# Performance work log

Hardware: AMD Instinct MI355X
Metric: run time of the kernel (lower is better)

The kernel has to match this reference:

```python
import jax, jax.numpy as jnp
import numpy as np

B, C, N = 16, 128, 2048  # batch, channels (SA_Layer(128)), num points


def setup_inputs() -> dict:
    key = jax.random.key(0)
    ks = jax.random.split(key, 6)
    x = jax.random.normal(ks[0], (B, C, N), jnp.float32)
    wq = jax.random.normal(ks[1], (C // 4, C), jnp.float32) * 0.05  # shared q/k 1x1 conv, no bias
    wv = jax.random.normal(ks[2], (C, C), jnp.float32) * 0.05
    bv = jax.random.normal(ks[3], (C,), jnp.float32) * 0.05
    wt = jax.random.normal(ks[4], (C, C), jnp.float32) * 0.05
    bt = jax.random.normal(ks[5], (C,), jnp.float32) * 0.05
    gamma = jnp.ones((C,), jnp.float32)   # BatchNorm1d weight
    beta = jnp.zeros((C,), jnp.float32)   # BatchNorm1d bias
    bn_mean = jnp.zeros((C,), jnp.float32)  # running mean (eval mode)
    bn_var = jnp.ones((C,), jnp.float32)    # running var (eval mode)
    return dict(x=x, wq=wq, wv=wv, bv=bv, wt=wt, bt=bt,
                gamma=gamma, beta=beta, bn_mean=bn_mean, bn_var=bn_var)


def reference(x, wq, wv, bv, wt, bt, gamma, beta, bn_mean, bn_var):
    EPS = 1e-9
    BN_EPS = 1e-5
    # q_conv and k_conv share weights (tied in __init__)
    x_q = jnp.einsum('dc,bcn->bnd', wq, x)               # [B, N, C/4]
    x_k = jnp.einsum('dc,bcn->bdn', wq, x)               # [B, C/4, N]
    energy = jnp.einsum('bnd,bdm->bnm', x_q, x_k)        # [B, N, N]
    attn = jax.nn.softmax(energy, axis=-1)
    # offset-attention renormalization: divide by column sum
    attn = attn / (EPS + attn.sum(axis=1, keepdims=True))
    x_v = jnp.einsum('dc,bcn->bdn', wv, x) + bv[None, :, None]   # [B, C, N]
    x_r = jnp.einsum('bdn,bnm->bdm', x_v, attn)                  # [B, C, N]
    t = jnp.einsum('dc,bcn->bdn', wt, x - x_r) + bt[None, :, None]
    # BatchNorm1d (eval mode) + ReLU
    t = (t - bn_mean[None, :, None]) * jax.lax.rsqrt(bn_var + BN_EPS)[None, :, None]
    t = t * gamma[None, :, None] + beta[None, :, None]
    return x + jax.nn.relu(t)
```

## Files before the change

### kernel.cpp

```cpp
#include <hip/hip_runtime.h>
#include <hip/hip_bf16.h>
#include <math.h>

#define BB 16
#define CC 128
#define NN 2048
#define CQ 32

typedef __attribute__((ext_vector_type(8))) short bf16x8;
typedef __attribute__((ext_vector_type(4))) float f32x4;
typedef __attribute__((ext_vector_type(16))) float f32x16;
typedef unsigned char uchar;

__device__ __forceinline__ ushort f2b(float f) {
    __hip_bfloat16 h = __float2bfloat16(f);
    return *reinterpret_cast<ushort*>(&h);
}
__device__ __forceinline__ float b2f(ushort u) {
    union { unsigned u; float f; } v; v.u = ((unsigned)u) << 16;
    return v.f;
}
__device__ __forceinline__ uint f2q4(float a, float b, float c, float d) {
    int r = __builtin_amdgcn_cvt_pk_fp8_f32(a, b, 0, false);
    r = __builtin_amdgcn_cvt_pk_fp8_f32(c, d, r, true);
    return (uint)r;
}
__device__ __forceinline__ bf16x8 as_b8(uint4 u) {
    union { uint4 u; bf16x8 b; } v; v.u = u; return v.b;
}
__device__ __forceinline__ bf16x8 as_b8_2(uint2 a, uint2 b) {
    return as_b8(make_uint4(a.x, a.y, b.x, b.y));
}
__device__ __forceinline__ float fexp2(float x) {
    return __builtin_amdgcn_exp2f(x);
}
union U2L { uint2 u; long l; };

#define OFF_VB  524288
#define OFF_RSI 4718592

#define QSCALE 1.2011224087864498f

__global__ __launch_bounds__(256) void k_proj(const float* __restrict__ x,
        const float* __restrict__ wq, const float* __restrict__ wv,
        const float* __restrict__ bv, ushort* __restrict__ Qt, uchar* __restrict__ Vb) {
    __shared__ ushort Wl[160][136];
    __shared__ ushort Xs[64][136];
    int bid = (blockIdx.x & 7) * 64 + (blockIdx.x >> 3);
    int b  = bid >> 5;
    int n0 = (bid & 31) << 6;
    int tid = threadIdx.x;
    #pragma unroll
    for (int k = 0; k < 20; ++k) {
        int idx = k * 256 + tid;
        int r = idx >> 5, c4 = (idx & 31) << 2;
        const float* srcw = (r < 32) ? (wq + r * 128 + c4) : (wv + (r - 32) * 128 + c4);
        float4 w4 = *(const float4*)srcw;
        float s = (r < 32) ? QSCALE : 1.0f;
        *(ushort4*)&Wl[r][c4] = make_ushort4(f2b(w4.x * s), f2b(w4.y * s),
                                             f2b(w4.z * s), f2b(w4.w * s));
    }
    const float* xb = x + (size_t)b * CC * NN;
    for (int idx = tid; idx < 2048; idx += 256) {
        int c = idx >> 4, n4 = (idx & 15) << 2;
        float4 xv = *(const float4*)&xb[c * NN + n0 + n4];
        Xs[n4][c]     = f2b(xv.x);
        Xs[n4 + 1][c] = f2b(xv.y);
        Xs[n4 + 2][c] = f2b(xv.z);
        Xs[n4 + 3][c] = f2b(xv.w);
    }
    __syncthreads();
    int w = tid >> 6, l = tid & 63, lr = l & 15, lg = l >> 4;
    f32x4 zero = {0.f, 0.f, 0.f, 0.f};
    int nn = n0 + w * 16 + lr;
    for (int dt = 0; dt < 10; ++dt) {
        f32x4 acc = zero;
        #pragma unroll
        for (int k = 0; k < 4; ++k) {
            bf16x8 a  = *(const bf16x8*)&Wl[dt * 16 + lr][k * 32 + lg * 8];
            bf16x8 bx = *(const bf16x8*)&Xs[w * 16 + lr][k * 32 + lg * 8];
            acc = __builtin_amdgcn_mfma_f32_16x16x32_bf16(a, bx, acc, 0, 0, 0);
        }
        if (dt < 2) {
            ushort4 p = make_ushort4(f2b(acc[0]), f2b(acc[1]), f2b(acc[2]), f2b(acc[3]));
            *(ushort4*)&Qt[(size_t)(b * NN + nn) * CQ + dt * 16 + lg * 4] = p;
        } else {
            union { uint u; uchar c[4]; } q;
            int vd = (dt - 2) * 16 + lg * 4;
            q.u = f2q4(acc[0] + bv[vd], acc[1] + bv[vd + 1],
                       acc[2] + bv[vd + 2], acc[3] + bv[vd + 3]);
            #pragma unroll
            for (int i = 0; i < 4; ++i)
                Vb[(size_t)(b * CC + vd + i) * NN + nn] = q.c[i];
        }
    }
}

__global__ __launch_bounds__(512) void k_rowstats(const ushort* __restrict__ Qt,
        float* __restrict__ RSI) {
    __shared__ ushort Qm[128][36];
    __shared__ float Sred[2][64];
    int bid = (blockIdx.x & 7) * 64 + (blockIdx.x >> 3);
    int b  = bid >> 5;
    int n0 = (bid & 31) << 6;
    int tid = threadIdx.x;
    int w = tid >> 6, l = tid & 63, lr = l & 15, lg = l >> 4;
    int wn = w & 3, wm = w >> 2;
    const ushort* Qtb = Qt + (size_t)b * NN * CQ;
    bf16x8 aq = *(const bf16x8*)&Qtb[(size_t)(n0 + wn * 16 + lr) * CQ + lg * 8];
    int sr = tid >> 2, sc = (tid & 3) * 8;
    uint4 q0 = *(const uint4*)&Qtb[(size_t)sr * CQ + sc];
    float S[4] = {0.f, 0.f, 0.f, 0.f};
    f32x4 zero = {0.f, 0.f, 0.f, 0.f};
    for (int t = 0; t < 16; ++t) {
        __syncthreads();
        *(uint4*)&Qm[sr][sc] = q0;
        __syncthreads();
        if (t < 15)
            q0 = *(const uint4*)&Qtb[(size_t)((t + 1) * 128 + sr) * CQ + sc];
        #pragma unroll
        for (int mi = 0; mi < 4; ++mi) {
            bf16x8 bq = *(const bf16x8*)&Qm[(wm * 4 + mi) * 16 + lr][lg * 8];
            f32x4 e = __builtin_amdgcn_mfma_f32_16x16x32_bf16(aq, bq, zero, 0, 0, 0);
            S[0] += fexp2(e[0]); S[1] += fexp2(e[1]);
            S[2] += fexp2(e[2]); S[3] += fexp2(e[3]);
        }
    }
    #pragma unroll
    for (int d = 1; d < 16; d <<= 1) {
        #pragma unroll
        for (int i = 0; i < 4; ++i) S[i] += __shfl_xor(S[i], d);
    }
    if (lr == 0) {
        #pragma unroll
        for (int i = 0; i < 4; ++i) Sred[wm][wn * 16 + lg * 4 + i] = S[i];
    }
    __syncthreads();
    if (tid < 64)
        RSI[b * NN + n0 + tid] = 256.f / (Sred[0][tid] + Sred[1][tid]);
}

__global__ __launch_bounds__(768, 3) void k_attn_pv(const ushort* __restrict__ Qt,
        const uchar* __restrict__ Vb, const float* __restrict__ RSI,
        const float* __restrict__ x, const float* __restrict__ wt,
        const float* __restrict__ bt, const float* __restrict__ gamma,
        const float* __restrict__ beta, const float* __restrict__ bn_mean,
        const float* __restrict__ bn_var, float* __restrict__ out) {
    __shared__ uchar SMp[2][2][128][72];
    __shared__ ushort wtl[16896];
    __shared__ float csred[4][128];
    __shared__ float csum[128];
    __shared__ float fAl[128], fBl[128];
    int bid = (blockIdx.x & 7) * 32 + (blockIdx.x >> 3);
    int b  = bid >> 4;
    int m0 = (bid & 15) << 7;
    int tid = threadIdx.x;
    int w = tid >> 6, l = tid & 63, lr = l & 15, lg = l >> 4;
    const ushort* Qtb = Qt + (size_t)b * NN * CQ;
    const uchar*  Vbb = Vb + (size_t)b * CC * NN;
    const float*  RSb = RSI + (size_t)b * NN;
    const float*  xb  = x   + (size_t)b * CC * NN;
    float*        outb = out + (size_t)b * CC * NN;
    f32x4 zero = {0.f, 0.f, 0.f, 0.f};
    bool producer = (w < 8);

    for (int idx = tid; idx < 4096; idx += 768) {
        int r = idx >> 5, c4 = (idx & 31) << 2;
        float4 w4 = *(const float4*)&wt[r * 128 + c4];
        *(ushort4*)&wtl[r * 132 + c4] =
            make_ushort4(f2b(w4.x), f2b(w4.y), f2b(w4.z), f2b(w4.w));
    }
    if (tid < 128) {
        float A = gamma[tid] * rsqrtf(bn_var[tid] + 1e-5f);
        fAl[tid] = A;
        fBl[tid] = (bt[tid] - bn_mean[tid]) * A + beta[tid];
    }

    int wn = w & 3, mh = w >> 2;
    bf16x8 bm[4];
    float cs[4] = {0.f, 0.f, 0.f, 0.f};
    int sv = 0, shv = 0;
    const uchar* vsrc = nullptr;
    bf16x8 aq_nx; float4 rsi_nx;
    int cw = w - 8;
    int dh = cw >> 1, mh2 = cw & 1;
    int ar = l & 31, kh = l >> 5;
    f32x16 pacc00, pacc01, pacc10, pacc11;

    if (producer) {
        #pragma unroll
        for (int mi = 0; mi < 4; ++mi)
            bm[mi] = *(const bf16x8*)&Qtb[(size_t)(m0 + (mh * 4 + mi) * 16 + lr) * CQ + lg * 8];
        sv = tid >> 2; shv = (tid & 3) * 16;
        vsrc = Vbb + (size_t)sv * NN + shv;
        {
            uint4 v0 = *(const uint4*)(vsrc);
            uchar* dst = &SMp[0][0][sv][shv];
            *(uint2*)(dst)     = make_uint2(v0.x, v0.y);
            *(uint2*)(dst + 8) = make_uint2(v0.z, v0.w);
        }
        {
            bf16x8 aq0 = *(const bf16x8*)&Qtb[(size_t)(wn * 16 + lr) * CQ + lg * 8];
            float4 r4 = *(const float4*)&RSb[wn * 16 + lg * 4];
            int nb = wn * 16 + lg * 4;
            #pragma unroll
            for (int mi = 0; mi < 4; ++mi) {
                f32x4 e = __builtin_amdgcn_mfma_f32_16x16x32_bf16(aq0, bm[mi], zero, 0, 0, 0);
                float w0 = fexp2(e[0]) * r4.x;
                float w1 = fexp2(e[1]) * r4.y;
                float w2 = fexp2(e[2]) * r4.z;
                float w3 = fexp2(e[3]) * r4.w;
                cs[mi] += w0 + w1 + w2 + w3;
                *(uint*)&SMp[1][0][(mh * 4 + mi) * 16 + lr][nb] = f2q4(w0, w1, w2, w3);
            }
        }
        aq_nx  = *(const bf16x8*)&Qtb[(size_t)(64 + wn * 16 + lr) * CQ + lg * 8];
        rsi_nx = *(const float4*)&RSb[64 + wn * 16 + lg * 4];
    } else {
        #pragma unroll
        for (int r = 0; r < 16; ++r) {
            pacc00[r] = 0.f; pacc01[r] = 0.f; pacc10[r] = 0.f; pacc11[r] = 0.f;
        }
    }
    __syncthreads();
    for (int t = 0; t < 32; ++t) {
        int cur = t & 1;
        if (producer) {
            if (t < 31) {
                int ntn = (t + 1) * 64;
                uint4 v0 = *(const uint4*)(vsrc + ntn);
                bf16x8 aq = aq_nx;
                float4 r4 = rsi_nx;
                if (t < 30) {
                    int nt2 = (t + 2) * 64;
                    aq_nx  = *(const bf16x8*)&Qtb[(size_t)(nt2 + wn * 16 + lr) * CQ + lg * 8];
                    rsi_nx = *(const float4*)&RSb[nt2 + wn * 16 + lg * 4];
                }
                int nb = wn * 16 + lg * 4;
                #pragma unroll
                for (int mi = 0; mi < 4; ++mi) {
                    f32x4 e = __builtin_amdgcn_mfma_f32_16x16x32_bf16(aq, bm[mi], zero, 0, 0, 0);
                    float w0 = fexp2(e[0]) * r4.x;
                    float w1 = fexp2(e[1]) * r4.y;
                    float w2 = fexp2(e[2]) * r4.z;
                    float w3 = fexp2(e[3]) * r4.w;
                    cs[mi] += w0 + w1 + w2 + w3;
                    *(uint*)&SMp[1][cur ^ 1][(mh * 4 + mi) * 16 + lr][nb] =
                        f2q4(w0, w1, w2, w3);
                }
                uchar* dst = &SMp[0][cur ^ 1][sv][shv];
                *(uint2*)(dst)     = make_uint2(v0.x, v0.y);
                *(uint2*)(dst + 8) = make_uint2(v0.z, v0.w);
            }
        } else {
            __builtin_amdgcn_s_setprio(1);
            #pragma unroll
            for (int kk = 0; kk < 4; ++kk) {
                int cb = kk * 16 + kh * 8;
                U2L va0, va1, wb0, wb1;
                va0.u = *(const uint2*)&SMp[0][cur][dh * 64 + ar][cb];
                va1.u = *(const uint2*)&SMp[0][cur][dh * 64 + 32 + ar][cb];
                wb0.u = *(const uint2*)&SMp[1][cur][mh2 * 64 + ar][cb];
                wb1.u = *(const uint2*)&SMp[1][cur][mh2 * 64 + 32 + ar][cb];
                pacc00 = __builtin_amdgcn_mfma_f32_32x32x16_fp8_fp8(va0.l, wb0.l, pacc00, 0, 0, 0);
                pacc01 = __builtin_amdgcn_mfma_f32_32x32x16_fp8_fp8(va0.l, wb1.l, pacc01, 0, 0, 0);
                pacc10 = __builtin_amdgcn_mfma_f32_32x32x16_fp8_fp8(va1.l, wb0.l, pacc10, 0, 0, 0);
                pacc11 = __builtin_amdgcn_mfma_f32_32x32x16_fp8_fp8(va1.l, wb1.l, pacc11, 0, 0, 0);
            }
            __builtin_amdgcn_s_setprio(0);
        }
        __syncthreads();
    }
    if (producer) {
        #pragma unroll
        for (int mi = 0; mi < 4; ++mi) {
            cs[mi] += __shfl_xor(cs[mi], 16);
            cs[mi] += __shfl_xor(cs[mi], 32);
        }
        if (lg == 0) {
            #pragma unroll
            for (int mi = 0; mi < 4; ++mi)
                csred[wn][(mh * 4 + mi) * 16 + lr] = cs[mi];
        }
    }
    __syncthreads();
    if (tid < 128) {
        float tot = csred[0][tid] + csred[1][tid] + csred[2][tid] + csred[3][tid];
        csum[tid] = 1.f / (2.56e-7f + tot);
    }
    __syncthreads();
    ushort* UsP = (ushort*)&SMp[0][0][0][0];
    if (!producer) {
        float inv0 = csum[mh2 * 64 + ar];
        float inv1 = csum[mh2 * 64 + 32 + ar];
        int mA = m0 + mh2 * 64 + ar;
        int mL = mh2 * 64 + ar;
        #pragma unroll
        for (int g = 0; g < 4; ++g) {
            int db = dh * 64 + 8 * g + 4 * kh;
            ushort4 u00, u01, u10, u11;
            #pragma unroll
            for (int j = 0; j < 4; ++j) {
                int r = 4 * g + j;
                float x00 = xb[(size_t)(db + j) * NN + mA];
                float x01 = xb[(size_t)(db + j) * NN + mA + 32];
                float x10 = xb[(size_t)(db + 32 + j) * NN + mA];
                float x11 = xb[(size_t)(db + 32 + j) * NN + mA + 32];
                ((ushort*)&u00)[j] = f2b(x00 - pacc00[r] * inv0);
                ((ushort*)&u01)[j] = f2b(x01 - pacc01[r] * inv1);
                ((ushort*)&u10)[j] = f2b(x10 - pacc10[r] * inv0);
                ((ushort*)&u11)[j] = f2b(x11 - pacc11[r] * inv1);
            }
            *(ushort4*)&UsP[mL * 132 + db]             = u00;
            *(ushort4*)&UsP[(mL + 32) * 132 + db]      = u01;
            *(ushort4*)&UsP[mL * 132 + db + 32]        = u10;
            *(ushort4*)&UsP[(mL + 32) * 132 + db + 32] = u11;
        }
    }
    __syncthreads();
    for (int tile = w; tile < 16; tile += 12) {
        int rt = tile >> 2, mt = tile & 3;
        f32x16 acc;
        #pragma unroll
        for (int r = 0; r < 16; ++r) acc[r] = 0.f;
        #pragma unroll
        for (int kk = 0; kk < 8; ++kk) {
            const ushort* ap = &wtl[(rt * 32 + ar) * 132 + kk * 16 + kh * 8];
            uint2 a0 = *(const uint2*)ap; uint2 a1 = *(const uint2*)(ap + 4);
            const ushort* bp = &UsP[(mt * 32 + ar) * 132 + kk * 16 + kh * 8];
            uint2 b0 = *(const uint2*)bp; uint2 b1 = *(const uint2*)(bp + 4);
            acc = __builtin_amdgcn_mfma_f32_32x32x16_bf16(
                as_b8_2(a0, a1), as_b8_2(b0, b1), acc, 0, 0, 0);
        }
        int m = m0 + mt * 32 + ar;
        #pragma unroll
        for (int g = 0; g < 4; ++g) {
            #pragma unroll
            for (int j = 0; j < 4; ++j) {
                int r = rt * 32 + j + 8 * g + 4 * kh;
                float t = acc[4 * g + j] * fAl[r] + fBl[r];
                t = fmaxf(t, 0.f);
                outb[(size_t)r * NN + m] = xb[(size_t)r * NN + m] + t;
            }
        }
    }
}

extern "C" void kernel_launch(void* const* d_in, const int* in_sizes, int n_in,
                              void* d_out, int out_size, void* d_ws, size_t ws_size,
                              hipStream_t stream) {
    const float* x       = (const float*)d_in[0];
    const float* wq      = (const float*)d_in[1];
    const float* wv      = (const float*)d_in[2];
    const float* bv      = (const float*)d_in[3];
    const float* wt      = (const float*)d_in[4];
    const float* bt      = (const float*)d_in[5];
    const float* gamma   = (const float*)d_in[6];
    const float* beta    = (const float*)d_in[7];
    const float* bn_mean = (const float*)d_in[8];
    const float* bn_var  = (const float*)d_in[9];
    float* out = (float*)d_out;
    float* ws  = (float*)d_ws;

    ushort* Qt   = (ushort*)ws;
    uchar*  Vbp  = (uchar*)(ws + OFF_VB);
    float*  RSI  = ws + OFF_RSI;

    k_proj<<<BB * 32, 256, 0, stream>>>(x, wq, wv, bv, Qt, Vbp);
    k_rowstats<<<BB * 32, 512, 0, stream>>>(Qt, RSI);
    k_attn_pv<<<BB * 16, 768, 0, stream>>>(Qt, Vbp, RSI, x, wt, bt, gamma, beta,
                                           bn_mean, bn_var, out);
}
```

Before: 57.09 us.

## Widen attention-PV block to 16 waves with 8 consumer waves

Raises the k_attn_pv block from 12 to 16 waves so there are 8 consumer waves instead of 4. Each consumer now covers a 32x128 output slice with two accumulators, down from 64x128 with four, which halves per-wave MFMA work and register pressure. The final Wt GEMM stage maps one tile to each of the 16 waves. The cost is more threads per block, so fewer blocks may fit per CU, and barrier synchronization spans more waves.

```diff
diff --git a/kernel.cpp b/kernel.cpp
--- a/kernel.cpp
+++ b/kernel.cpp
@@ -140,7 +140,7 @@
         RSI[b * NN + n0 + tid] = 256.f / (Sred[0][tid] + Sred[1][tid]);
 }
 
-__global__ __launch_bounds__(768, 3) void k_attn_pv(const ushort* __restrict__ Qt,
+__global__ __launch_bounds__(1024, 4) void k_attn_pv(const ushort* __restrict__ Qt,
         const uchar* __restrict__ Vb, const float* __restrict__ RSI,
         const float* __restrict__ x, const float* __restrict__ wt,
         const float* __restrict__ bt, const float* __restrict__ gamma,
@@ -164,7 +164,7 @@
     f32x4 zero = {0.f, 0.f, 0.f, 0.f};
     bool producer = (w < 8);
 
-    for (int idx = tid; idx < 4096; idx += 768) {
+    for (int idx = tid; idx < 4096; idx += 1024) {
         int r = idx >> 5, c4 = (idx & 31) << 2;
         float4 w4 = *(const float4*)&wt[r * 128 + c4];
         *(ushort4*)&wtl[r * 132 + c4] =
@@ -183,9 +183,9 @@
     const uchar* vsrc = nullptr;
     bf16x8 aq_nx; float4 rsi_nx;
     int cw = w - 8;
-    int dh = cw >> 1, mh2 = cw & 1;
+    int dq = cw >> 1, mh2 = cw & 1;
     int ar = l & 31, kh = l >> 5;
-    f32x16 pacc00, pacc01, pacc10, pacc11;
+    f32x16 pacc0, pacc1;
 
     if (producer) {
         #pragma unroll
@@ -218,9 +218,7 @@
         rsi_nx = *(const float4*)&RSb[64 + wn * 16 + lg * 4];
     } else {
         #pragma unroll
-        for (int r = 0; r < 16; ++r) {
-            pacc00[r] = 0.f; pacc01[r] = 0.f; pacc10[r] = 0.f; pacc11[r] = 0.f;
-        }
+        for (int r = 0; r < 16; ++r) { pacc0[r] = 0.f; pacc1[r] = 0.f; }
     }
     __syncthreads();
     for (int t = 0; t < 32; ++t) {
@@ -257,15 +255,12 @@
             #pragma unroll
             for (int kk = 0; kk < 4; ++kk) {
                 int cb = kk * 16 + kh * 8;
-                U2L va0, va1, wb0, wb1;
-                va0.u = *(const uint2*)&SMp[0][cur][dh * 64 + ar][cb];
-                va1.u = *(const uint2*)&SMp[0][cur][dh * 64 + 32 + ar][cb];
+                U2L va, wb0, wb1;
+                va.u  = *(const uint2*)&SMp[0][cur][dq * 32 + ar][cb];
                 wb0.u = *(const uint2*)&SMp[1][cur][mh2 * 64 + ar][cb];
                 wb1.u = *(const uint2*)&SMp[1][cur][mh2 * 64 + 32 + ar][cb];
-                pacc00 = __builtin_amdgcn_mfma_f32_32x32x16_fp8_fp8(va0.l, wb0.l, pacc00, 0, 0, 0);
-                pacc01 = __builtin_amdgcn_mfma_f32_32x32x16_fp8_fp8(va0.l, wb1.l, pacc01, 0, 0, 0);
-                pacc10 = __builtin_amdgcn_mfma_f32_32x32x16_fp8_fp8(va1.l, wb0.l, pacc10, 0, 0, 0);
-                pacc11 = __builtin_amdgcn_mfma_f32_32x32x16_fp8_fp8(va1.l, wb1.l, pacc11, 0, 0, 0);
+                pacc0 = __builtin_amdgcn_mfma_f32_32x32x16_fp8_fp8(va.l, wb0.l, pacc0, 0, 0, 0);
+                pacc1 = __builtin_amdgcn_mfma_f32_32x32x16_fp8_fp8(va.l, wb1.l, pacc1, 0, 0, 0);
             }
             __builtin_amdgcn_s_setprio(0);
         }
@@ -297,28 +292,23 @@
         int mL = mh2 * 64 + ar;
         #pragma unroll
         for (int g = 0; g < 4; ++g) {
-            int db = dh * 64 + 8 * g + 4 * kh;
-            ushort4 u00, u01, u10, u11;
+            int db = dq * 32 + 8 * g + 4 * kh;
+            ushort4 u0, u1;
             #pragma unroll
             for (int j = 0; j < 4; ++j) {
                 int r = 4 * g + j;
-                float x00 = xb[(size_t)(db + j) * NN + mA];
-                float x01 = xb[(size_t)(db + j) * NN + mA + 32];
-                float x10 = xb[(size_t)(db + 32 + j) * NN + mA];
-                float x11 = xb[(size_t)(db + 32 + j) * NN + mA + 32];
-                ((ushort*)&u00)[j] = f2b(x00 - pacc00[r] * inv0);
-                ((ushort*)&u01)[j] = f2b(x01 - pacc01[r] * inv1);
-                ((ushort*)&u10)[j] = f2b(x10 - pacc10[r] * inv0);
-                ((ushort*)&u11)[j] = f2b(x11 - pacc11[r] * inv1);
-            }
-            *(ushort4*)&UsP[mL * 132 + db]             = u00;
-            *(ushort4*)&UsP[(mL + 32) * 132 + db]      = u01;
-            *(ushort4*)&UsP[mL * 132 + db + 32]        = u10;
-            *(ushort4*)&UsP[(mL + 32) * 132 + db + 32] = u11;
-        }
-    }
-    __syncthreads();
-    for (int tile = w; tile < 16; tile += 12) {
+                float x0 = xb[(size_t)(db + j) * NN + mA];
+                float x1 = xb[(size_t)(db + j) * NN + mA + 32];
+                ((ushort*)&u0)[j] = f2b(x0 - pacc0[r] * inv0);
+                ((ushort*)&u1)[j] = f2b(x1 - pacc1[r] * inv1);
+            }
+            *(ushort4*)&UsP[mL * 132 + db]        = u0;
+            *(ushort4*)&UsP[(mL + 32) * 132 + db] = u1;
+        }
+    }
+    __syncthreads();
+    {
+        int tile = w;
         int rt = tile >> 2, mt = tile & 3;
         f32x16 acc;
         #pragma unroll
@@ -368,6 +358,6 @@
 
     k_proj<<<BB * 32, 256, 0, stream>>>(x, wq, wv, bv, Qt, Vbp);
     k_rowstats<<<BB * 32, 512, 0, stream>>>(Qt, RSI);
-    k_attn_pv<<<BB * 16, 768, 0, stream>>>(Qt, Vbp, RSI, x, wt, bt, gamma, beta,
-                                           bn_mean, bn_var, out);
-}
+    k_attn_pv<<<BB * 16, 1024, 0, stream>>>(Qt, Vbp, RSI, x, wt, bt, gamma, beta,
+                                            bn_mean, bn_var, out);
+}
```

Result: no change. 56.40 us (-1.2%).
